# Kernel tuning notes

Hardware: AMD Instinct MI355X
Metric: run time of the kernel (lower is better)

## Reference

```python
import jax, jax.numpy as jnp
import numpy as np


def _chamfer_single_directional(x, y):
    """Mean over batch of mean over points of min_j ||x_i - y_j||^2.

    x: [B, N, 3] (predicted), y: [B, M, 3] (target).
    Matches pytorch3d chamfer_distance(x, y, single_directional=True)
    with norm=2, point_reduction='mean', batch_reduction='mean'.
    """
    x2 = jnp.sum(x * x, axis=-1)                      # [B, N]
    y2 = jnp.sum(y * y, axis=-1)                      # [B, M]
    cross = jnp.einsum('bnd,bmd->bnm', x, y)          # [B, N, M]
    d2 = x2[:, :, None] + y2[:, None, :] - 2.0 * cross  # squared L2
    min_d2 = jnp.min(d2, axis=2)                      # [B, N] nearest in y
    return jnp.mean(jnp.mean(min_d2, axis=1))         # scalar


def setup_inputs() -> dict:
    key = jax.random.key(0)
    k1, k2 = jax.random.split(key)
    v = jax.random.normal(k1, (4, 8192, 3), dtype=jnp.float32)
    v_pred = jax.random.normal(k2, (4, 8192, 3), dtype=jnp.float32)
    return {"v": v, "v_pred": v_pred}


def reference(v, v_pred):
    # forward: chamfer_distance(v_pred, v, single_directional=True)
    return _chamfer_single_directional(v_pred, v)
```

## Files before the change

### kernel.cpp

```cpp
#include <hip/hip_runtime.h>

#define BB 4
#define NN 8192
#define MM 8192
#define BN (BB * NN)

#define BLK 256
#define P   8
#define NX  (BLK*P)
#define S   64
#define MC  (MM/S)

#define KEY_C 128.0f

typedef float v2f __attribute__((ext_vector_type(2)));

#if defined(__has_builtin) && __has_builtin(__builtin_elementwise_fma)
#define VFMA(a, b, c) __builtin_elementwise_fma((a), (b), (c))
#else
static __device__ inline v2f VFMA(v2f a, v2f b, v2f c) {
    v2f r; r.x = __builtin_fmaf(a.x, b.x, c.x); r.y = __builtin_fmaf(a.y, b.y, c.y);
    return r;
}
#endif

__global__ __launch_bounds__(BLK) void chamfer_min_atomic(
    const float* __restrict__ y,
    const float* __restrict__ x,
    int* __restrict__ gkey)
{
    __shared__ __attribute__((aligned(16))) float ZX[MC];
    __shared__ __attribute__((aligned(16))) float ZY[MC];
    __shared__ __attribute__((aligned(16))) float ZZ[MC];
    __shared__ __attribute__((aligned(16))) float ZW[MC];

    const int t  = threadIdx.x;
    const int ib = blockIdx.x;
    const int s  = blockIdx.y;
    const int b  = blockIdx.z;

    const float* yb = y + ((size_t)b * MM + (size_t)s * MC) * 3;
    if (t < MC) {
        float y0 = yb[3*t + 0];
        float y1 = yb[3*t + 1];
        float y2 = yb[3*t + 2];
        ZX[t] = 2.0f * y0;
        ZY[t] = 2.0f * y1;
        ZZ[t] = 2.0f * y2;
        ZW[t] = __builtin_fmaf(y2, y2, __builtin_fmaf(y1, y1, y0*y0));
    }
    __syncthreads();

    float nx0[P], nx1[P], nx2[P], xx[P], best[P];
    const float* xb = x + ((size_t)b * NN + (size_t)ib * NX) * 3;
#pragma unroll
    for (int p = 0; p < P; ++p) {
        int i = t + p * BLK;
        float a0 = xb[3*i + 0];
        float a1 = xb[3*i + 1];
        float a2 = xb[3*i + 2];
        nx0[p] = -a0; nx1[p] = -a1; nx2[p] = -a2;
        xx[p] = __builtin_fmaf(a2, a2, __builtin_fmaf(a1, a1, a0*a0));
        best[p] = 3.4e38f;
    }

#pragma unroll 2
    for (int jj = 0; jj < MC; jj += 4) {
        float4 ax = ((const float4*)ZX)[jj >> 2];
        float4 ay = ((const float4*)ZY)[jj >> 2];
        float4 az = ((const float4*)ZZ)[jj >> 2];
        float4 aw = ((const float4*)ZW)[jj >> 2];
        v2f zx01 = {ax.x, ax.y}, zx23 = {ax.z, ax.w};
        v2f zy01 = {ay.x, ay.y}, zy23 = {ay.z, ay.w};
        v2f zz01 = {az.x, az.y}, zz23 = {az.z, az.w};
        v2f zw01 = {aw.x, aw.y}, zw23 = {aw.z, aw.w};
#pragma unroll
        for (int p = 0; p < P; ++p) {
            v2f s0 = {nx0[p], nx0[p]};
            v2f s1 = {nx1[p], nx1[p]};
            v2f s2 = {nx2[p], nx2[p]};
            v2f t01 = VFMA(s0, zx01, zw01);
            t01 = VFMA(s1, zy01, t01);
            t01 = VFMA(s2, zz01, t01);
            v2f t23 = VFMA(s0, zx23, zw23);
            t23 = VFMA(s1, zy23, t23);
            t23 = VFMA(s2, zz23, t23);
            float m3 = fminf(fminf(t01.x, t01.y), t23.x);
            best[p] = fminf(fminf(m3, t23.y), best[p]);
        }
    }

    int* gk = gkey + (size_t)b * NN + (size_t)ib * NX;
#pragma unroll
    for (int p = 0; p < P; ++p) {
        float d2  = best[p] + xx[p];
        float key = KEY_C - d2;
        atomicMax(&gk[t + p * BLK], __float_as_int(key));
    }
}

__global__ __launch_bounds__(1024) void final_sum(
    const int* __restrict__ gkey,
    float* __restrict__ out)
{
    const int t = threadIdx.x;
    const int4* g4 = (const int4*)gkey;
    float acc = 0.0f;
#pragma unroll
    for (int i = t; i < BN / 4; i += 1024) {
        int4 k = g4[i];
        acc += (KEY_C - __int_as_float(k.x)) + (KEY_C - __int_as_float(k.y))
             + (KEY_C - __int_as_float(k.z)) + (KEY_C - __int_as_float(k.w));
    }
    for (int off = 32; off > 0; off >>= 1) {
        acc += __shfl_down(acc, off, 64);
    }
    __shared__ float wsum[16];
    const int lane = t & 63;
    const int w    = t >> 6;
    if (lane == 0) wsum[w] = acc;
    __syncthreads();
    if (t == 0) {
        float tot = 0.0f;
#pragma unroll
        for (int i = 0; i < 16; ++i) tot += wsum[i];
        out[0] = tot * (1.0f / (float)BN);
    }
}

extern "C" void kernel_launch(void* const* d_in, const int* in_sizes, int n_in,
                              void* d_out, int out_size, void* d_ws, size_t ws_size,
                              hipStream_t stream) {
    const float* v      = (const float*)d_in[0];
    const float* v_pred = (const float*)d_in[1];
    float* out = (float*)d_out;

    int* gkey = (int*)d_ws;

    dim3 grid1(NN / NX, S, BB);
    chamfer_min_atomic<<<grid1, BLK, 0, stream>>>(v, v_pred, gkey);

    final_sum<<<1, 1024, 0, stream>>>(gkey, out);
}
```

Measured before the change: 76.66 us.

## Compute chamfer distances with split-bf16 MFMA matrix instructions

Replaces the scalar FMA distance loop with bf16 MFMA 32x32x16 instructions. The operands are split into hi/lo bf16 pairs and packed with norm and bias terms so one matrix product yields KEY_C minus the squared distance directly. Running maxima are kept in the accumulator layout, reduced across lanes with shuffles, and merged across blocks with atomicMax. The goal is to move the O(NM) work onto matrix cores; the cost is bf16 split precision error, which may change the result slightly compared with fp32.

```diff
diff --git a/kernel.cpp b/kernel.cpp
--- a/kernel.cpp
+++ b/kernel.cpp
@@ -6,96 +6,118 @@
 #define BN (BB * NN)
 
 #define BLK 256
-#define P   8
-#define NX  (BLK*P)
-#define S   64
-#define MC  (MM/S)
+#define QB  256
+#define TC  1024
+#define SCH (MM / TC)
+#define NJT (TC / 32)
 
 #define KEY_C 128.0f
 
-typedef float v2f __attribute__((ext_vector_type(2)));
+typedef __bf16 bf16x8 __attribute__((ext_vector_type(8)));
+typedef float  f32x16 __attribute__((ext_vector_type(16)));
 
-#if defined(__has_builtin) && __has_builtin(__builtin_elementwise_fma)
-#define VFMA(a, b, c) __builtin_elementwise_fma((a), (b), (c))
-#else
-static __device__ inline v2f VFMA(v2f a, v2f b, v2f c) {
-    v2f r; r.x = __builtin_fmaf(a.x, b.x, c.x); r.y = __builtin_fmaf(a.y, b.y, c.y);
-    return r;
+
+static __device__ inline void split_bf(float v, __bf16& h, __bf16& l) {
+    h = (__bf16)v;
+    l = (__bf16)(v - (float)h);
 }
-#endif
 
-__global__ __launch_bounds__(BLK) void chamfer_min_atomic(
+__global__ __launch_bounds__(BLK, 4) void chamfer_mfma(
     const float* __restrict__ y,
     const float* __restrict__ x,
     int* __restrict__ gkey)
 {
-    __shared__ __attribute__((aligned(16))) float ZX[MC];
-    __shared__ __attribute__((aligned(16))) float ZY[MC];
-    __shared__ __attribute__((aligned(16))) float ZZ[MC];
-    __shared__ __attribute__((aligned(16))) float ZW[MC];
+    __shared__ uint4 FR[NJT * 64];
 
     const int t  = threadIdx.x;
+    const int l  = t & 63;
+    const int w  = t >> 6;
     const int ib = blockIdx.x;
     const int s  = blockIdx.y;
     const int b  = blockIdx.z;
 
-    const float* yb = y + ((size_t)b * MM + (size_t)s * MC) * 3;
-    if (t < MC) {
-        float y0 = yb[3*t + 0];
-        float y1 = yb[3*t + 1];
-        float y2 = yb[3*t + 2];
-        ZX[t] = 2.0f * y0;
-        ZY[t] = 2.0f * y1;
-        ZZ[t] = 2.0f * y2;
-        ZW[t] = __builtin_fmaf(y2, y2, __builtin_fmaf(y1, y1, y0*y0));
+    {
+        const float* xb = x + ((size_t)b * NN + (size_t)ib * QB) * 3;
+        float x0 = xb[3*t+0], x1 = xb[3*t+1], x2 = xb[3*t+2];
+        __bf16 h0,l0,h1,l1,h2,l2;
+        split_bf(2.0f*x0, h0, l0);
+        split_bf(2.0f*x1, h1, l1);
+        split_bf(2.0f*x2, h2, l2);
+        float nxx = -__builtin_fmaf(x2, x2, __builtin_fmaf(x1, x1, x0*x0));
+        __bf16 hx, lx; split_bf(nxx, hx, lx);
+        const __bf16 one = (__bf16)1.0f;
+        bf16x8 g0 = {h0,h0,l0,l0,h1,h1,l1,l1};
+        bf16x8 g1 = {h2,h2,l2,l2,hx,lx,one,one};
+        const int at = t >> 5, col = t & 31;
+        FR[at*64 +      col] = __builtin_bit_cast(uint4, g0);
+        FR[at*64 + 32 + col] = __builtin_bit_cast(uint4, g1);
+    }
+    __syncthreads();
+    const uint4 afr0 = FR[(w*2 + 0)*64 + l];
+    const uint4 afr1 = FR[(w*2 + 1)*64 + l];
+    __syncthreads();
+
+    {
+        const float* yb = y + ((size_t)b * MM + (size_t)s * TC) * 3;
+        const __bf16 one = (__bf16)1.0f;
+#pragma unroll
+        for (int k2 = 0; k2 < 4; ++k2) {
+            const int j = t + k2 * BLK;
+            float y0 = yb[3*j+0], y1 = yb[3*j+1], y2 = yb[3*j+2];
+            __bf16 h0,l0,h1,l1,h2,l2;
+            split_bf(y0, h0, l0);
+            split_bf(y1, h1, l1);
+            split_bf(y2, h2, l2);
+            float nyy = -__builtin_fmaf(y2, y2, __builtin_fmaf(y1, y1, y0*y0));
+            __bf16 hy, ly; split_bf(nyy, hy, ly);
+            bf16x8 g0 = {h0,l0,h0,l0,h1,l1,h1,l1};
+            bf16x8 g1 = {h2,l2,h2,l2,one,one,hy,ly};
+            const int jt = j >> 5, col = j & 31;
+            FR[jt*64 +      col] = __builtin_bit_cast(uint4, g0);
+            FR[jt*64 + 32 + col] = __builtin_bit_cast(uint4, g1);
+        }
     }
     __syncthreads();
 
-    float nx0[P], nx1[P], nx2[P], xx[P], best[P];
-    const float* xb = x + ((size_t)b * NN + (size_t)ib * NX) * 3;
+    f32x16 ck;
 #pragma unroll
-    for (int p = 0; p < P; ++p) {
-        int i = t + p * BLK;
-        float a0 = xb[3*i + 0];
-        float a1 = xb[3*i + 1];
-        float a2 = xb[3*i + 2];
-        nx0[p] = -a0; nx1[p] = -a1; nx2[p] = -a2;
-        xx[p] = __builtin_fmaf(a2, a2, __builtin_fmaf(a1, a1, a0*a0));
-        best[p] = 3.4e38f;
+    for (int r = 0; r < 16; ++r) ck[r] = KEY_C;
+    f32x16 best0, best1;
+#pragma unroll
+    for (int r = 0; r < 16; ++r) { best0[r] = -3.4e38f; best1[r] = -3.4e38f; }
+
+    const bf16x8 a0 = __builtin_bit_cast(bf16x8, afr0);
+    const bf16x8 a1 = __builtin_bit_cast(bf16x8, afr1);
+
+#pragma unroll 2
+    for (int jt = 0; jt < NJT; ++jt) {
+        const bf16x8 bf = __builtin_bit_cast(bf16x8, FR[jt*64 + l]);
+        f32x16 acc0 = __builtin_amdgcn_mfma_f32_32x32x16_bf16(a0, bf, ck, 0, 0, 0);
+        f32x16 acc1 = __builtin_amdgcn_mfma_f32_32x32x16_bf16(a1, bf, ck, 0, 0, 0);
+#pragma unroll
+        for (int r = 0; r < 16; ++r) best0[r] = fmaxf(best0[r], acc0[r]);
+#pragma unroll
+        for (int r = 0; r < 16; ++r) best1[r] = fmaxf(best1[r], acc1[r]);
     }
 
-#pragma unroll 2
-    for (int jj = 0; jj < MC; jj += 4) {
-        float4 ax = ((const float4*)ZX)[jj >> 2];
-        float4 ay = ((const float4*)ZY)[jj >> 2];
-        float4 az = ((const float4*)ZZ)[jj >> 2];
-        float4 aw = ((const float4*)ZW)[jj >> 2];
-        v2f zx01 = {ax.x, ax.y}, zx23 = {ax.z, ax.w};
-        v2f zy01 = {ay.x, ay.y}, zy23 = {ay.z, ay.w};
-        v2f zz01 = {az.x, az.y}, zz23 = {az.z, az.w};
-        v2f zw01 = {aw.x, aw.y}, zw23 = {aw.z, aw.w};
+    int* gk = gkey + (size_t)b * NN + (size_t)ib * QB;
+    const int g = l >> 5;
 #pragma unroll
-        for (int p = 0; p < P; ++p) {
-            v2f s0 = {nx0[p], nx0[p]};
-            v2f s1 = {nx1[p], nx1[p]};
-            v2f s2 = {nx2[p], nx2[p]};
-            v2f t01 = VFMA(s0, zx01, zw01);
-            t01 = VFMA(s1, zy01, t01);
-            t01 = VFMA(s2, zz01, t01);
-            v2f t23 = VFMA(s0, zx23, zw23);
-            t23 = VFMA(s1, zy23, t23);
-            t23 = VFMA(s2, zz23, t23);
-            float m3 = fminf(fminf(t01.x, t01.y), t23.x);
-            best[p] = fminf(fminf(m3, t23.y), best[p]);
+    for (int ii = 0; ii < 2; ++ii) {
+        const f32x16 bb = ii ? best1 : best0;
+#pragma unroll
+        for (int r = 0; r < 16; ++r) {
+            float v = bb[r];
+            v = fmaxf(v, __shfl_xor(v, 1, 64));
+            v = fmaxf(v, __shfl_xor(v, 2, 64));
+            v = fmaxf(v, __shfl_xor(v, 4, 64));
+            v = fmaxf(v, __shfl_xor(v, 8, 64));
+            v = fmaxf(v, __shfl_xor(v, 16, 64));
+            if ((l & 31) == 0) {
+                const int row = (r & 3) + 8 * (r >> 2) + 4 * g;
+                atomicMax(&gk[(w*2 + ii)*32 + row], __float_as_int(v));
+            }
         }
-    }
-
-    int* gk = gkey + (size_t)b * NN + (size_t)ib * NX;
-#pragma unroll
-    for (int p = 0; p < P; ++p) {
-        float d2  = best[p] + xx[p];
-        float key = KEY_C - d2;
-        atomicMax(&gk[t + p * BLK], __float_as_int(key));
     }
 }
 
@@ -137,8 +159,8 @@
 
     int* gkey = (int*)d_ws;
 
-    dim3 grid1(NN / NX, S, BB);
-    chamfer_min_atomic<<<grid1, BLK, 0, stream>>>(v, v_pred, gkey);
+    dim3 grid1(NN / QB, SCH, BB);
+    chamfer_mfma<<<grid1, BLK, 0, stream>>>(v, v_pred, gkey);
 
     final_sum<<<1, 1024, 0, stream>>>(gkey, out);
 }
```

Result: faster. 72.55 us (-5.4%).
